# Performance work log

Measured on AMD Instinct MI355X. Metric: run time of the kernel, lower is better.

## Reference

```python
import jax, jax.numpy as jnp
import numpy as np

B, S, H, Q = 32, 128, 128, 3  # users, seq_len, hidden_size, quadkey_level
L = Q - 1  # number of mixing scales


def setup_inputs() -> dict:
    key = jax.random.key(0)
    ks = jax.random.split(key, 12)
    trend0 = jax.random.normal(ks[0], (B, S, H), dtype=jnp.float32)
    trend1 = jax.random.normal(ks[1], (B, S, H), dtype=jnp.float32)
    trend2 = jax.random.normal(ks[2], (B, S, H), dtype=jnp.float32)
    # Per-position prefix linears padded into dense tensors, zero-masked beyond
    # the prefix length j+1 so the ragged math is exact:
    #   W1[j, :j+1, :j+1] ~ Linear(j+1, j+1), b1[j, :j+1]
    #   W2[j, :j+1]      ~ Linear(j+1, 1),   b2[j]
    idx = jnp.arange(S)
    pm = (idx[None, :] <= idx[:, None]).astype(jnp.float32)  # [j, s]: s <= j
    W1 = jax.random.normal(ks[3], (L, S, S, S), dtype=jnp.float32) * 0.05
    W1 = W1 * pm[None, :, :, None] * pm[None, :, None, :]
    b1 = jax.random.normal(ks[4], (L, S, S), dtype=jnp.float32) * 0.05 * pm[None]
    W2 = jax.random.normal(ks[5], (L, S, S), dtype=jnp.float32) * 0.05 * pm[None]
    b2 = jax.random.normal(ks[6], (L, S), dtype=jnp.float32) * 0.05
    # shared output MLP: Linear(H,H)->GELU->Linear(H,H); stored as [in, out]
    Wm1 = jax.random.normal(ks[7], (H, H), dtype=jnp.float32) * 0.05
    bm1 = jax.random.normal(ks[8], (H,), dtype=jnp.float32) * 0.05
    Wm2 = jax.random.normal(ks[9], (H, H), dtype=jnp.float32) * 0.05
    bm2 = jax.random.normal(ks[10], (H,), dtype=jnp.float32) * 0.05
    return {"trend0": trend0, "trend1": trend1, "trend2": trend2,
            "W1": W1, "b1": b1, "W2": W2, "b2": b2,
            "Wm1": Wm1, "bm1": bm1, "Wm2": Wm2, "bm2": bm2}


def reference(trend0, trend1, trend2, W1, b1, W2, b2, Wm1, bm1, Wm2, bm2):
    gelu = lambda x: jax.nn.gelu(x, approximate=False)  # torch nn.GELU default
    mlp = lambda x: gelu(x @ Wm1 + bm1) @ Wm2 + bm2

    rev = [trend2, trend1, trend0]  # trend_list reversed
    out_low = rev[0]
    out_high = rev[1]
    outs = [out_low]
    for i in range(Q - 1):
        # vectorized ragged prefix mix: per position j, out_low[:, :j+1] (as [B,H,j+1])
        # -> Linear(j+1,j+1) -> GELU -> Linear(j+1,1). Zero-padding in W1/b1/W2
        # kills all contributions beyond the prefix (GELU(0)=0).
        y1 = jnp.einsum('bsh,jst->bhjt', out_low, W1[i]) + b1[i]  # [B,H,S,S]
        res = jnp.einsum('bhjt,jt->bjh', gelu(y1), W2[i]) + b2[i][None, :, None]
        out_high = out_high + res
        out_low = out_high
        if i + 2 <= Q - 1:
            out_high = rev[i + 2]
        out_low = mlp(out_low)
        outs.append(out_low)
    outs.reverse()
    return tuple(outs)
```

## Files before the change

### kernel.cpp

```cpp
#include <hip/hip_runtime.h>
#include <stdint.h>

#define BSH (32 * 128 * 128)

typedef __attribute__((ext_vector_type(8))) __bf16 bf16x8;
typedef __attribute__((ext_vector_type(4))) float f32x4;

__device__ __forceinline__ unsigned short f2bf(float f) {
  union { float f; unsigned u; } v; v.f = f;
  return (unsigned short)((v.u + 0x7FFFu + ((v.u >> 16) & 1u)) >> 16);
}

__device__ __forceinline__ float fast_exp2(float x) {
#if __has_builtin(__builtin_amdgcn_exp2f)
  return __builtin_amdgcn_exp2f(x);
#else
  float r; asm("v_exp_f32 %0, %1" : "=v"(r) : "v"(x)); return r;
#endif
}
__device__ __forceinline__ float fast_rcp(float x) {
#if __has_builtin(__builtin_amdgcn_rcpf)
  return __builtin_amdgcn_rcpf(x);
#else
  float r; asm("v_rcp_f32 %0, %1" : "=v"(r) : "v"(x)); return r;
#endif
}

__device__ __forceinline__ float gelu_f(float y) {
  float u = y * y;
  float p = __builtin_fmaf(u, 0.044715f, 1.0f) * y;
  float w = fast_exp2(p * 2.30220787f);
  return y - y * fast_rcp(1.0f + w);
}


__device__ __forceinline__ void transpose_block_c(const float* __restrict__ src,
                                                  unsigned short* __restrict__ dst,
                                                  unsigned short* lds) {
  const int tid = threadIdx.x;
  const float4* s4 = (const float4*)src;
#pragma unroll
  for (int it = 0; it < 16; ++it) {
    int i4 = tid + it * 256;
    float4 v = s4[i4];
    int s = i4 >> 5;
    int t0 = (i4 * 4) & 127;
    int sc = s >> 3, se = s & 7;
#pragma unroll
    for (int e = 0; e < 4; ++e) {
      int t = t0 + e;
      lds[t * 136 + ((sc ^ ((t >> 2) & 7)) << 3) + se] = f2bf(((const float*)&v)[e]);
    }
  }
  __syncthreads();
#pragma unroll
  for (int it = 0; it < 8; ++it) {
    int c = tid + it * 256;
    int tr = c >> 4, sc = c & 15;
    uint4 d = *(const uint4*)(lds + tr * 136 + ((sc ^ ((tr >> 2) & 7)) << 3));
    *(uint4*)(dst + (sc * 128 + tr) * 8) = d;
  }
}

__global__ __launch_bounds__(256) void prepass_kernel(
    const float* __restrict__ W1, const float* __restrict__ trend2,
    const float* __restrict__ Wm1, const float* __restrict__ Wm2,
    unsigned short* __restrict__ W1Tc, unsigned short* __restrict__ T2c,
    unsigned short* __restrict__ Wm1c, unsigned short* __restrict__ Wm2c,
    float* __restrict__ out2) {
  __shared__ unsigned short lds[128 * 136];
  const int bid = blockIdx.x;
  if (bid < 256) {
    transpose_block_c(W1 + bid * 16384, W1Tc + bid * 16384, lds);
  } else if (bid < 288) {
    const int b = bid - 256;
    transpose_block_c(trend2 + b * 16384, T2c + b * 16384, lds);
    const float4* s4 = (const float4*)(trend2 + b * 16384);
    float4* d4 = (float4*)(out2 + b * 16384);
#pragma unroll
    for (int it = 0; it < 16; ++it)
      d4[threadIdx.x + it * 256] = s4[threadIdx.x + it * 256];
  } else if (bid == 288) {
    transpose_block_c(Wm1, Wm1c, lds);
  } else {
    transpose_block_c(Wm2, Wm2c, lds);
  }
}

__global__ __launch_bounds__(256, 4) void mix_kernel(
    const unsigned short* __restrict__ XTc,
    const unsigned short* __restrict__ W1Tc,
    const float* __restrict__ b1,
    const float* __restrict__ W2,
    const float* __restrict__ b2,
    const float* __restrict__ trend,
    unsigned short* __restrict__ xoutc) {
  __shared__ float res_ws[4][4][64];
  const int bid = blockIdx.x;
  const int jg = bid >> 5;
  const int b = bid & 31;
  const int j0 = jg * 4;
  const int tid = threadIdx.x;
  const int wave = tid >> 6;
  const int lane = tid & 63;
  const int lane15 = lane & 15;
  const int quad = lane >> 4;

  const int ntiles = (j0 >> 4) + 1;
  const int ksteps = (j0 >> 5) + 1;

  const unsigned short* Bb = XTc + b * 16384;
  const unsigned short* A0 = W1Tc + j0 * 16384;
  const float C = -2.45546937f;

#pragma unroll
  for (int p = 0; p < 2; ++p) {
    float psum[4][4];
#pragma unroll
    for (int jj = 0; jj < 4; ++jj)
#pragma unroll
      for (int ni = 0; ni < 4; ++ni) psum[jj][ni] = 0.f;

#pragma unroll
    for (int q = 0; q < 2; ++q) {
      const int mt = wave + q * 4;
      if (mt < ntiles) {
        f32x4 acc[4][4];
#pragma unroll
        for (int jj = 0; jj < 4; ++jj)
#pragma unroll
          for (int ni = 0; ni < 4; ++ni) {
            f32x4 z = {0.f, 0.f, 0.f, 0.f};
            acc[jj][ni] = z;
          }
        for (int ks = 0; ks < ksteps; ++ks) {
          const int kq = ks * 4 + quad;
          const unsigned short* bp = Bb + (kq * 128 + p * 64 + lane15) * 8;
          bf16x8 bf0 = *(const bf16x8*)(bp);
          bf16x8 bf1 = *(const bf16x8*)(bp + 128);
          bf16x8 bf2 = *(const bf16x8*)(bp + 256);
          bf16x8 bf3 = *(const bf16x8*)(bp + 384);
#pragma unroll
          for (int jj = 0; jj < 4; ++jj) {
            bf16x8 a = *(const bf16x8*)(A0 + jj * 16384 +
                                        (kq * 128 + mt * 16 + lane15) * 8);
            acc[jj][0] = __builtin_amdgcn_mfma_f32_16x16x32_bf16(a, bf0, acc[jj][0], 0, 0, 0);
            acc[jj][1] = __builtin_amdgcn_mfma_f32_16x16x32_bf16(a, bf1, acc[jj][1], 0, 0, 0);
            acc[jj][2] = __builtin_amdgcn_mfma_f32_16x16x32_bf16(a, bf2, acc[jj][2], 0, 0, 0);
            acc[jj][3] = __builtin_amdgcn_mfma_f32_16x16x32_bf16(a, bf3, acc[jj][3], 0, 0, 0);
          }
        }
        const int tb = mt * 16 + quad * 4;
#pragma unroll
        for (int jj = 0; jj < 4; ++jj) {
          const int j = j0 + jj;
          float4 b1v = *(const float4*)(b1 + j * 128 + tb);
          float4 w2v = *(const float4*)(W2 + j * 128 + tb);
#pragma unroll
          for (int r = 0; r < 4; ++r) {
            float b1r = ((const float*)&b1v)[r];
            float w2r = ((const float*)&w2v)[r];
            float cb = C * b1r;
            float bw = b1r * w2r;
#pragma unroll
            for (int ni = 0; ni < 4; ++ni) {
              float a = acc[jj][ni][r];
              float m = __builtin_fmaf(a, C, cb);
              float e = fast_exp2(m);
              float rr = fast_rcp(1.0f + e);
              float yw = __builtin_fmaf(a, w2r, bw);
              psum[jj][ni] = __builtin_fmaf(yw, rr, psum[jj][ni]);
            }
          }
        }
      }
    }
#pragma unroll
    for (int jj = 0; jj < 4; ++jj)
#pragma unroll
      for (int ni = 0; ni < 4; ++ni) {
        float v = psum[jj][ni];
        v += __shfl_xor(v, 16, 64);
        v += __shfl_xor(v, 32, 64);
        psum[jj][ni] = v;
      }
#pragma unroll
    for (int jj = 0; jj < 4; ++jj)
      res_ws[wave][jj][quad * 16 + lane15] = psum[jj][quad];
    __syncthreads();
    {
      const int jj = tid >> 6;
      const int hh = tid & 63;
      const int j = j0 + jj;
      const int h = p * 64 + hh;
      float v = res_ws[0][jj][hh] + res_ws[1][jj][hh] +
                res_ws[2][jj][hh] + res_ws[3][jj][hh] +
                b2[j] + trend[(b * 128 + j) * 128 + h];
      xoutc[b * 16384 + ((h >> 3) * 128 + j) * 8 + (h & 7)] = f2bf(v);
    }
    __syncthreads();
  }
}

__global__ __launch_bounds__(256) void mlp_kernel(
    const unsigned short* __restrict__ Xc,
    const unsigned short* __restrict__ Wm1c,
    const unsigned short* __restrict__ Wm2c,
    const float* __restrict__ bm1,
    const float* __restrict__ bm2,
    float* __restrict__ outf,
    unsigned short* __restrict__ outTc,
    const int write_t) {
  __shared__ __align__(16) unsigned short U[16 * 128];
  __shared__ unsigned short ldsT[16 * 136];
  const int bid = blockIdx.x;
  const int b = bid >> 3;
  const int mb = bid & 7;
  const int tid = threadIdx.x;
  const int wave = tid >> 6;
  const int lane = tid & 63;
  const int lane15 = lane & 15;
  const int quad = lane >> 4;

  const unsigned short* Xb = Xc + b * 16384;

  f32x4 acc[2];
  { f32x4 z = {0.f, 0.f, 0.f, 0.f}; acc[0] = z; acc[1] = z; }
#pragma unroll
  for (int ks = 0; ks < 4; ++ks) {
    int kq = ks * 4 + quad;
    bf16x8 a  = *(const bf16x8*)(Xb + (kq * 128 + mb * 16 + lane15) * 8);
    bf16x8 w0 = *(const bf16x8*)(Wm1c + (kq * 128 + wave * 32 + lane15) * 8);
    bf16x8 w1 = *(const bf16x8*)(Wm1c + (kq * 128 + wave * 32 + 16 + lane15) * 8);
    acc[0] = __builtin_amdgcn_mfma_f32_16x16x32_bf16(a, w0, acc[0], 0, 0, 0);
    acc[1] = __builtin_amdgcn_mfma_f32_16x16x32_bf16(a, w1, acc[1], 0, 0, 0);
  }
#pragma unroll
  for (int ni = 0; ni < 2; ++ni) {
    int n = wave * 32 + ni * 16 + lane15;
    float bv = bm1[n];
#pragma unroll
    for (int r = 0; r < 4; ++r) {
      int jr = quad * 4 + r;
      U[((n >> 3) * 16 + jr) * 8 + (n & 7)] = f2bf(gelu_f(acc[ni][r] + bv));
    }
  }
  __syncthreads();
  { f32x4 z = {0.f, 0.f, 0.f, 0.f}; acc[0] = z; acc[1] = z; }
#pragma unroll
  for (int ks = 0; ks < 4; ++ks) {
    int kq = ks * 4 + quad;
    bf16x8 a  = *(const bf16x8*)(U + (kq * 16 + lane15) * 8);
    bf16x8 w0 = *(const bf16x8*)(Wm2c + (kq * 128 + wave * 32 + lane15) * 8);
    bf16x8 w1 = *(const bf16x8*)(Wm2c + (kq * 128 + wave * 32 + 16 + lane15) * 8);
    acc[0] = __builtin_amdgcn_mfma_f32_16x16x32_bf16(a, w0, acc[0], 0, 0, 0);
    acc[1] = __builtin_amdgcn_mfma_f32_16x16x32_bf16(a, w1, acc[1], 0, 0, 0);
  }
  {
    float* outb = outf + b * 16384 + mb * 16 * 128;
#pragma unroll
    for (int ni = 0; ni < 2; ++ni) {
      int n = wave * 32 + ni * 16 + lane15;
      float bv = bm2[n];
#pragma unroll
      for (int r = 0; r < 4; ++r) {
        int jr = quad * 4 + r;
        float v = acc[ni][r] + bv;
        outb[jr * 128 + n] = v;
        if (write_t) ldsT[jr * 136 + n] = f2bf(v);
      }
    }
  }
  if (write_t) {
    __syncthreads();
    int h = tid & 127, jr8 = tid >> 7;
    unsigned short tmp[8] __attribute__((aligned(16)));
#pragma unroll
    for (int e = 0; e < 8; ++e) tmp[e] = ldsT[(jr8 * 8 + e) * 136 + h];
    *(uint4*)(outTc + b * 16384 + ((mb * 2 + jr8) * 128 + h) * 8) = *(const uint4*)tmp;
  }
}

extern "C" void kernel_launch(void* const* d_in, const int* in_sizes, int n_in,
                              void* d_out, int out_size, void* d_ws, size_t ws_size,
                              hipStream_t stream) {
  (void)in_sizes; (void)n_in; (void)out_size; (void)ws_size;
  const float* trend0 = (const float*)d_in[0];
  const float* trend1 = (const float*)d_in[1];
  const float* trend2 = (const float*)d_in[2];
  const float* W1  = (const float*)d_in[3];
  const float* b1  = (const float*)d_in[4];
  const float* W2  = (const float*)d_in[5];
  const float* b2  = (const float*)d_in[6];
  const float* Wm1 = (const float*)d_in[7];
  const float* bm1 = (const float*)d_in[8];
  const float* Wm2 = (const float*)d_in[9];
  const float* bm2 = (const float*)d_in[10];
  float* out = (float*)d_out;
  char* ws = (char*)d_ws;

  unsigned short* W1Tc = (unsigned short*)(ws);
  unsigned short* T2c  = (unsigned short*)(ws + 8388608);
  unsigned short* x1c  = (unsigned short*)(ws + 9437184);
  unsigned short* A1Tc = (unsigned short*)(ws + 10485760);
  unsigned short* x2c  = (unsigned short*)(ws + 11534336);
  unsigned short* Wm1c = (unsigned short*)(ws + 12582912);
  unsigned short* Wm2c = (unsigned short*)(ws + 12615680);

  prepass_kernel<<<290, 256, 0, stream>>>(W1, trend2, Wm1, Wm2,
                                          W1Tc, T2c, Wm1c, Wm2c, out + 2 * BSH);
  mix_kernel<<<1024, 256, 0, stream>>>(T2c, W1Tc, b1, W2, b2, trend1, x1c);
  mlp_kernel<<<256, 256, 0, stream>>>(x1c, Wm1c, Wm2c, bm1, bm2,
                                      out + BSH, A1Tc, 1);
  mix_kernel<<<1024, 256, 0, stream>>>(A1Tc, W1Tc + 128 * 16384, b1 + 16384,
                                       W2 + 16384, b2 + 128, trend0, x2c);
  mlp_kernel<<<256, 256, 0, stream>>>(x2c, Wm1c, Wm2c, bm1, bm2,
                                      out, (unsigned short*)nullptr, 0);
}
```

Measured before the change: 146.5 us.

## Fuse output MLP into mix kernel and rebalance ragged block order

Folds the shared output MLP into the mix kernel. Each block keeps its 4 mixed rows in LDS and runs both MLP GEMMs on a 16-row tile that is zero-padded and only 4 rows full, which removes two launches and the intermediate bf16 round trip through global memory. Blocks now map to j-groups in a zig-zag order so the triangular, ragged work is spread more evenly across the grid, and the prepass W1 transpose uses the same ordering. The cost is padded MFMA work on the MLP (only a quarter of each tile is used), smaller output stores, and extra LDS per block, which may affect occupancy.

```diff
diff --git a/kernel.cpp b/kernel.cpp
--- a/kernel.cpp
+++ b/kernel.cpp
@@ -33,6 +33,9 @@
   return y - y * fast_rcp(1.0f + w);
 }
 
+__device__ __forceinline__ int jg_of(int x, int cls) {
+  return cls == 0 ? x : cls == 1 ? 15 - x : cls == 2 ? 16 + x : 31 - x;
+}
 
 __device__ __forceinline__ void transpose_block_c(const float* __restrict__ src,
                                                   unsigned short* __restrict__ dst,
@@ -71,7 +74,11 @@
   __shared__ unsigned short lds[128 * 136];
   const int bid = blockIdx.x;
   if (bid < 256) {
-    transpose_block_c(W1 + bid * 16384, W1Tc + bid * 16384, lds);
+    int x = bid & 7, r = bid >> 3;
+    int stage = r >> 4, rr = r & 15;
+    int j = jg_of(x, rr >> 2) * 4 + (rr & 3);
+    int blk = stage * 128 + j;
+    transpose_block_c(W1 + blk * 16384, W1Tc + blk * 16384, lds);
   } else if (bid < 288) {
     const int b = bid - 256;
     transpose_block_c(trend2 + b * 16384, T2c + b * 16384, lds);
@@ -87,18 +94,28 @@
   }
 }
 
-__global__ __launch_bounds__(256, 4) void mix_kernel(
+__global__ __launch_bounds__(256, 4) void mix_fused_kernel(
     const unsigned short* __restrict__ XTc,
-    const unsigned short* __restrict__ W1Tc,
-    const float* __restrict__ b1,
-    const float* __restrict__ W2,
-    const float* __restrict__ b2,
-    const float* __restrict__ trend,
-    unsigned short* __restrict__ xoutc) {
+    const unsigned short* __restrict__ W1Tj,
+    const float* __restrict__ b1j,
+    const float* __restrict__ W2j,
+    const float* __restrict__ b2j,
+    const float* __restrict__ trendR,
+    const unsigned short* __restrict__ Wm1c,
+    const unsigned short* __restrict__ Wm2c,
+    const float* __restrict__ bm1,
+    const float* __restrict__ bm2,
+    float* __restrict__ outF,
+    unsigned short* __restrict__ outTc,
+    const int write_t) {
   __shared__ float res_ws[4][4][64];
+  __shared__ __align__(16) unsigned short xa[16 * 128];
+  __shared__ __align__(16) unsigned short U[16 * 128];
   const int bid = blockIdx.x;
-  const int jg = bid >> 5;
-  const int b = bid & 31;
+  const int x = bid & 7;
+  const int i = bid >> 3;
+  const int b = i & 31;
+  const int jg = jg_of(x, i >> 5);
   const int j0 = jg * 4;
   const int tid = threadIdx.x;
   const int wave = tid >> 6;
@@ -106,11 +123,16 @@
   const int lane15 = lane & 15;
   const int quad = lane >> 4;
 
+  {
+    uint4 z = {0, 0, 0, 0};
+    ((uint4*)xa)[tid] = z;
+    ((uint4*)U)[tid] = z;
+  }
+
   const int ntiles = (j0 >> 4) + 1;
   const int ksteps = (j0 >> 5) + 1;
-
   const unsigned short* Bb = XTc + b * 16384;
-  const unsigned short* A0 = W1Tc + j0 * 16384;
+  const unsigned short* A0 = W1Tj + j0 * 16384;
   const float C = -2.45546937f;
 
 #pragma unroll
@@ -136,26 +158,27 @@
         for (int ks = 0; ks < ksteps; ++ks) {
           const int kq = ks * 4 + quad;
           const unsigned short* bp = Bb + (kq * 128 + p * 64 + lane15) * 8;
-          bf16x8 bf0 = *(const bf16x8*)(bp);
-          bf16x8 bf1 = *(const bf16x8*)(bp + 128);
-          bf16x8 bf2 = *(const bf16x8*)(bp + 256);
-          bf16x8 bf3 = *(const bf16x8*)(bp + 384);
-#pragma unroll
-          for (int jj = 0; jj < 4; ++jj) {
-            bf16x8 a = *(const bf16x8*)(A0 + jj * 16384 +
-                                        (kq * 128 + mt * 16 + lane15) * 8);
-            acc[jj][0] = __builtin_amdgcn_mfma_f32_16x16x32_bf16(a, bf0, acc[jj][0], 0, 0, 0);
-            acc[jj][1] = __builtin_amdgcn_mfma_f32_16x16x32_bf16(a, bf1, acc[jj][1], 0, 0, 0);
-            acc[jj][2] = __builtin_amdgcn_mfma_f32_16x16x32_bf16(a, bf2, acc[jj][2], 0, 0, 0);
-            acc[jj][3] = __builtin_amdgcn_mfma_f32_16x16x32_bf16(a, bf3, acc[jj][3], 0, 0, 0);
-          }
+          bf16x8 bfr[4], af[4];
+#pragma unroll
+          for (int ni = 0; ni < 4; ++ni)
+            bfr[ni] = *(const bf16x8*)(bp + ni * 128);
+#pragma unroll
+          for (int jj = 0; jj < 4; ++jj)
+            af[jj] = *(const bf16x8*)(A0 + jj * 16384 +
+                                      (kq * 128 + mt * 16 + lane15) * 8);
+#pragma unroll
+          for (int jj = 0; jj < 4; ++jj)
+#pragma unroll
+            for (int ni = 0; ni < 4; ++ni)
+              acc[jj][ni] = __builtin_amdgcn_mfma_f32_16x16x32_bf16(
+                  af[jj], bfr[ni], acc[jj][ni], 0, 0, 0);
         }
         const int tb = mt * 16 + quad * 4;
 #pragma unroll
         for (int jj = 0; jj < 4; ++jj) {
           const int j = j0 + jj;
-          float4 b1v = *(const float4*)(b1 + j * 128 + tb);
-          float4 w2v = *(const float4*)(W2 + j * 128 + tb);
+          float4 b1v = *(const float4*)(b1j + j * 128 + tb);
+          float4 w2v = *(const float4*)(W2j + j * 128 + tb);
 #pragma unroll
           for (int r = 0; r < 4; ++r) {
             float b1r = ((const float*)&b1v)[r];
@@ -167,9 +190,9 @@
               float a = acc[jj][ni][r];
               float m = __builtin_fmaf(a, C, cb);
               float e = fast_exp2(m);
-              float rr = fast_rcp(1.0f + e);
+              float rr2 = fast_rcp(1.0f + e);
               float yw = __builtin_fmaf(a, w2r, bw);
-              psum[jj][ni] = __builtin_fmaf(yw, rr, psum[jj][ni]);
+              psum[jj][ni] = __builtin_fmaf(yw, rr2, psum[jj][ni]);
             }
           }
         }
@@ -195,89 +218,62 @@
       const int h = p * 64 + hh;
       float v = res_ws[0][jj][hh] + res_ws[1][jj][hh] +
                 res_ws[2][jj][hh] + res_ws[3][jj][hh] +
-                b2[j] + trend[(b * 128 + j) * 128 + h];
-      xoutc[b * 16384 + ((h >> 3) * 128 + j) * 8 + (h & 7)] = f2bf(v);
+                b2j[j] + trendR[(b * 128 + j) * 128 + h];
+      xa[((h >> 3) * 16 + jj) * 8 + (h & 7)] = f2bf(v);
     }
     __syncthreads();
   }
-}
-
-__global__ __launch_bounds__(256) void mlp_kernel(
-    const unsigned short* __restrict__ Xc,
-    const unsigned short* __restrict__ Wm1c,
-    const unsigned short* __restrict__ Wm2c,
-    const float* __restrict__ bm1,
-    const float* __restrict__ bm2,
-    float* __restrict__ outf,
-    unsigned short* __restrict__ outTc,
-    const int write_t) {
-  __shared__ __align__(16) unsigned short U[16 * 128];
-  __shared__ unsigned short ldsT[16 * 136];
-  const int bid = blockIdx.x;
-  const int b = bid >> 3;
-  const int mb = bid & 7;
-  const int tid = threadIdx.x;
-  const int wave = tid >> 6;
-  const int lane = tid & 63;
-  const int lane15 = lane & 15;
-  const int quad = lane >> 4;
-
-  const unsigned short* Xb = Xc + b * 16384;
-
-  f32x4 acc[2];
-  { f32x4 z = {0.f, 0.f, 0.f, 0.f}; acc[0] = z; acc[1] = z; }
+
+  f32x4 acc2[2];
+  { f32x4 z = {0.f, 0.f, 0.f, 0.f}; acc2[0] = z; acc2[1] = z; }
 #pragma unroll
   for (int ks = 0; ks < 4; ++ks) {
     int kq = ks * 4 + quad;
-    bf16x8 a  = *(const bf16x8*)(Xb + (kq * 128 + mb * 16 + lane15) * 8);
-    bf16x8 w0 = *(const bf16x8*)(Wm1c + (kq * 128 + wave * 32 + lane15) * 8);
-    bf16x8 w1 = *(const bf16x8*)(Wm1c + (kq * 128 + wave * 32 + 16 + lane15) * 8);
-    acc[0] = __builtin_amdgcn_mfma_f32_16x16x32_bf16(a, w0, acc[0], 0, 0, 0);
-    acc[1] = __builtin_amdgcn_mfma_f32_16x16x32_bf16(a, w1, acc[1], 0, 0, 0);
-  }
-#pragma unroll
-  for (int ni = 0; ni < 2; ++ni) {
-    int n = wave * 32 + ni * 16 + lane15;
-    float bv = bm1[n];
-#pragma unroll
-    for (int r = 0; r < 4; ++r) {
-      int jr = quad * 4 + r;
-      U[((n >> 3) * 16 + jr) * 8 + (n & 7)] = f2bf(gelu_f(acc[ni][r] + bv));
+    bf16x8 a = *(const bf16x8*)(xa + (kq * 16 + lane15) * 8);
+    bf16x8 w0 = *(const bf16x8*)(Wm1c + (kq * 128 + (wave * 2 + 0) * 16 + lane15) * 8);
+    bf16x8 w1 = *(const bf16x8*)(Wm1c + (kq * 128 + (wave * 2 + 1) * 16 + lane15) * 8);
+    acc2[0] = __builtin_amdgcn_mfma_f32_16x16x32_bf16(a, w0, acc2[0], 0, 0, 0);
+    acc2[1] = __builtin_amdgcn_mfma_f32_16x16x32_bf16(a, w1, acc2[1], 0, 0, 0);
+  }
+  if (quad == 0) {
+#pragma unroll
+    for (int nt = 0; nt < 2; ++nt) {
+      int o = (wave * 2 + nt) * 16 + lane15;
+      float bv = bm1[o];
+#pragma unroll
+      for (int r = 0; r < 4; ++r) {
+        float g = gelu_f(acc2[nt][r] + bv);
+        U[((o >> 3) * 16 + r) * 8 + (o & 7)] = f2bf(g);
+      }
     }
   }
   __syncthreads();
-  { f32x4 z = {0.f, 0.f, 0.f, 0.f}; acc[0] = z; acc[1] = z; }
+  { f32x4 z = {0.f, 0.f, 0.f, 0.f}; acc2[0] = z; acc2[1] = z; }
 #pragma unroll
   for (int ks = 0; ks < 4; ++ks) {
     int kq = ks * 4 + quad;
-    bf16x8 a  = *(const bf16x8*)(U + (kq * 16 + lane15) * 8);
-    bf16x8 w0 = *(const bf16x8*)(Wm2c + (kq * 128 + wave * 32 + lane15) * 8);
-    bf16x8 w1 = *(const bf16x8*)(Wm2c + (kq * 128 + wave * 32 + 16 + lane15) * 8);
-    acc[0] = __builtin_amdgcn_mfma_f32_16x16x32_bf16(a, w0, acc[0], 0, 0, 0);
-    acc[1] = __builtin_amdgcn_mfma_f32_16x16x32_bf16(a, w1, acc[1], 0, 0, 0);
-  }
-  {
-    float* outb = outf + b * 16384 + mb * 16 * 128;
-#pragma unroll
-    for (int ni = 0; ni < 2; ++ni) {
-      int n = wave * 32 + ni * 16 + lane15;
-      float bv = bm2[n];
+    bf16x8 a = *(const bf16x8*)(U + (kq * 16 + lane15) * 8);
+    bf16x8 w0 = *(const bf16x8*)(Wm2c + (kq * 128 + (wave * 2 + 0) * 16 + lane15) * 8);
+    bf16x8 w1 = *(const bf16x8*)(Wm2c + (kq * 128 + (wave * 2 + 1) * 16 + lane15) * 8);
+    acc2[0] = __builtin_amdgcn_mfma_f32_16x16x32_bf16(a, w0, acc2[0], 0, 0, 0);
+    acc2[1] = __builtin_amdgcn_mfma_f32_16x16x32_bf16(a, w1, acc2[1], 0, 0, 0);
+  }
+  if (quad == 0) {
+#pragma unroll
+    for (int nt = 0; nt < 2; ++nt) {
+      int o = (wave * 2 + nt) * 16 + lane15;
+      float bv = bm2[o];
+      unsigned short tmp4[4] __attribute__((aligned(8)));
 #pragma unroll
       for (int r = 0; r < 4; ++r) {
-        int jr = quad * 4 + r;
-        float v = acc[ni][r] + bv;
-        outb[jr * 128 + n] = v;
-        if (write_t) ldsT[jr * 136 + n] = f2bf(v);
+        float v = acc2[nt][r] + bv;
+        outF[b * 16384 + (j0 + r) * 128 + o] = v;
+        tmp4[r] = f2bf(v);
       }
-    }
-  }
-  if (write_t) {
-    __syncthreads();
-    int h = tid & 127, jr8 = tid >> 7;
-    unsigned short tmp[8] __attribute__((aligned(16)));
-#pragma unroll
-    for (int e = 0; e < 8; ++e) tmp[e] = ldsT[(jr8 * 8 + e) * 136 + h];
-    *(uint4*)(outTc + b * 16384 + ((mb * 2 + jr8) * 128 + h) * 8) = *(const uint4*)tmp;
+      if (write_t)
+        *(uint2*)(outTc + b * 16384 + ((j0 >> 3) * 128 + o) * 8 + (j0 & 7)) =
+            *(const uint2*)tmp4;
+    }
   }
 }
 
@@ -301,19 +297,16 @@
 
   unsigned short* W1Tc = (unsigned short*)(ws);
   unsigned short* T2c  = (unsigned short*)(ws + 8388608);
-  unsigned short* x1c  = (unsigned short*)(ws + 9437184);
-  unsigned short* A1Tc = (unsigned short*)(ws + 10485760);
-  unsigned short* x2c  = (unsigned short*)(ws + 11534336);
-  unsigned short* Wm1c = (unsigned short*)(ws + 12582912);
-  unsigned short* Wm2c = (unsigned short*)(ws + 12615680);
+  unsigned short* A1Tc = (unsigned short*)(ws + 9437184);
+  unsigned short* Wm1c = (unsigned short*)(ws + 10485760);
+  unsigned short* Wm2c = (unsigned short*)(ws + 10518528);
 
   prepass_kernel<<<290, 256, 0, stream>>>(W1, trend2, Wm1, Wm2,
                                           W1Tc, T2c, Wm1c, Wm2c, out + 2 * BSH);
-  mix_kernel<<<1024, 256, 0, stream>>>(T2c, W1Tc, b1, W2, b2, trend1, x1c);
-  mlp_kernel<<<256, 256, 0, stream>>>(x1c, Wm1c, Wm2c, bm1, bm2,
-                                      out + BSH, A1Tc, 1);
-  mix_kernel<<<1024, 256, 0, stream>>>(A1Tc, W1Tc + 128 * 16384, b1 + 16384,
-                                       W2 + 16384, b2 + 128, trend0, x2c);
-  mlp_kernel<<<256, 256, 0, stream>>>(x2c, Wm1c, Wm2c, bm1, bm2,
-                                      out, (unsigned short*)nullptr, 0);
-}
+  mix_fused_kernel<<<1024, 256, 0, stream>>>(
+      T2c, W1Tc, b1, W2, b2, trend1, Wm1c, Wm2c, bm1, bm2,
+      out + BSH, A1Tc, 1);
+  mix_fused_kernel<<<1024, 256, 0, stream>>>(
+      A1Tc, W1Tc + 128 * 16384, b1 + 16384, W2 + 16384, b2 + 128, trend0,
+      Wm1c, Wm2c, bm1, bm2, out, (unsigned short*)nullptr, 0);
+}
```

Result: no change. 145.8 us (-0.5%).

## Pair small and large prefix positions per block to balance triangular mix work

Applied to the files above, without the earlier changes.

The mix kernel now gives each 128-thread block one batch and a pair of positions j and 127-j, so every block carries roughly the same amount of triangular work. Each wave owns one half of the hidden dimension and loops over all M tiles itself, which removes the cross-wave LDS reduction and the __syncthreads. The prepass also reorders which W1 blocks each workgroup transposes, pairing small and large positions there as well. In exchange the per-block parallelism is lower, since each wave iterates serially over up to eight tiles, and more blocks are launched.

```diff
diff --git a/kernel.cpp b/kernel.cpp
--- a/kernel.cpp
+++ b/kernel.cpp
@@ -32,7 +32,6 @@
   float w = fast_exp2(p * 2.30220787f);
   return y - y * fast_rcp(1.0f + w);
 }
-
 
 __device__ __forceinline__ void transpose_block_c(const float* __restrict__ src,
                                                   unsigned short* __restrict__ dst,
@@ -71,7 +70,13 @@
   __shared__ unsigned short lds[128 * 136];
   const int bid = blockIdx.x;
   if (bid < 256) {
-    transpose_block_c(W1 + bid * 16384, W1Tc + bid * 16384, lds);
+    int x = bid & 7, i = bid >> 3;
+    int stage = i >> 4, u = i & 15;
+    int m = u & 7, half = u >> 3;
+    int jpp = x + 8 * m;
+    int j = half ? 127 - jpp : jpp;
+    int blk = stage * 128 + j;
+    transpose_block_c(W1 + blk * 16384, W1Tc + blk * 16384, lds);
   } else if (bid < 288) {
     const int b = bid - 256;
     transpose_block_c(trend2 + b * 16384, T2c + b * 16384, lds);
@@ -87,118 +92,116 @@
   }
 }
 
-__global__ __launch_bounds__(256, 4) void mix_kernel(
+__global__ __launch_bounds__(128, 4) void mix_kernel(
     const unsigned short* __restrict__ XTc,
-    const unsigned short* __restrict__ W1Tc,
-    const float* __restrict__ b1,
-    const float* __restrict__ W2,
-    const float* __restrict__ b2,
-    const float* __restrict__ trend,
+    const unsigned short* __restrict__ W1Tj,
+    const float* __restrict__ b1j,
+    const float* __restrict__ W2j,
+    const float* __restrict__ b2j,
+    const float* __restrict__ trendR,
     unsigned short* __restrict__ xoutc) {
-  __shared__ float res_ws[4][4][64];
   const int bid = blockIdx.x;
-  const int jg = bid >> 5;
-  const int b = bid & 31;
-  const int j0 = jg * 4;
+  const int b = bid >> 6;
+  const int jp = bid & 63;
+  const int js = jp, jb = 127 - jp;
   const int tid = threadIdx.x;
-  const int wave = tid >> 6;
+  const int p = tid >> 6;
   const int lane = tid & 63;
   const int lane15 = lane & 15;
   const int quad = lane >> 4;
 
-  const int ntiles = (j0 >> 4) + 1;
-  const int ksteps = (j0 >> 5) + 1;
-
-  const unsigned short* Bb = XTc + b * 16384;
-  const unsigned short* A0 = W1Tc + j0 * 16384;
+  const int nt_s = (js >> 4) + 1, ks_s = (js >> 5) + 1;
+  const int nt_b = (jb >> 4) + 1, ks_b = (jb >> 5) + 1;
+
+  const unsigned short* Bp = XTc + b * 16384 + (p * 64 + lane15) * 8;
+  const unsigned short* As = W1Tj + js * 16384 + lane15 * 8;
+  const unsigned short* Ab = W1Tj + jb * 16384 + lane15 * 8;
   const float C = -2.45546937f;
 
-#pragma unroll
-  for (int p = 0; p < 2; ++p) {
-    float psum[4][4];
-#pragma unroll
-    for (int jj = 0; jj < 4; ++jj)
-#pragma unroll
-      for (int ni = 0; ni < 4; ++ni) psum[jj][ni] = 0.f;
-
-#pragma unroll
-    for (int q = 0; q < 2; ++q) {
-      const int mt = wave + q * 4;
-      if (mt < ntiles) {
-        f32x4 acc[4][4];
-#pragma unroll
-        for (int jj = 0; jj < 4; ++jj)
-#pragma unroll
-          for (int ni = 0; ni < 4; ++ni) {
-            f32x4 z = {0.f, 0.f, 0.f, 0.f};
-            acc[jj][ni] = z;
-          }
-        for (int ks = 0; ks < ksteps; ++ks) {
-          const int kq = ks * 4 + quad;
-          const unsigned short* bp = Bb + (kq * 128 + p * 64 + lane15) * 8;
-          bf16x8 bf0 = *(const bf16x8*)(bp);
-          bf16x8 bf1 = *(const bf16x8*)(bp + 128);
-          bf16x8 bf2 = *(const bf16x8*)(bp + 256);
-          bf16x8 bf3 = *(const bf16x8*)(bp + 384);
-#pragma unroll
-          for (int jj = 0; jj < 4; ++jj) {
-            bf16x8 a = *(const bf16x8*)(A0 + jj * 16384 +
-                                        (kq * 128 + mt * 16 + lane15) * 8);
-            acc[jj][0] = __builtin_amdgcn_mfma_f32_16x16x32_bf16(a, bf0, acc[jj][0], 0, 0, 0);
-            acc[jj][1] = __builtin_amdgcn_mfma_f32_16x16x32_bf16(a, bf1, acc[jj][1], 0, 0, 0);
-            acc[jj][2] = __builtin_amdgcn_mfma_f32_16x16x32_bf16(a, bf2, acc[jj][2], 0, 0, 0);
-            acc[jj][3] = __builtin_amdgcn_mfma_f32_16x16x32_bf16(a, bf3, acc[jj][3], 0, 0, 0);
-          }
+  float psum[2][4];
+#pragma unroll
+  for (int jj = 0; jj < 2; ++jj)
+#pragma unroll
+    for (int ni = 0; ni < 4; ++ni) psum[jj][ni] = 0.f;
+
+  for (int mt = 0; mt < nt_b; ++mt) {
+    const bool in_s = (mt < nt_s);
+    f32x4 acc[2][4];
+#pragma unroll
+    for (int jj = 0; jj < 2; ++jj)
+#pragma unroll
+      for (int ni = 0; ni < 4; ++ni) {
+        f32x4 z = {0.f, 0.f, 0.f, 0.f};
+        acc[jj][ni] = z;
+      }
+    const int mo = mt * 128;
+    for (int ks = 0; ks < ks_b; ++ks) {
+      const int ko = (ks * 4 + quad) * 1024;
+      bf16x8 vb0 = *(const bf16x8*)(Bp + ko);
+      bf16x8 vb1 = *(const bf16x8*)(Bp + ko + 128);
+      bf16x8 vb2 = *(const bf16x8*)(Bp + ko + 256);
+      bf16x8 vb3 = *(const bf16x8*)(Bp + ko + 384);
+      bf16x8 ab = *(const bf16x8*)(Ab + ko + mo);
+      acc[1][0] = __builtin_amdgcn_mfma_f32_16x16x32_bf16(ab, vb0, acc[1][0], 0, 0, 0);
+      acc[1][1] = __builtin_amdgcn_mfma_f32_16x16x32_bf16(ab, vb1, acc[1][1], 0, 0, 0);
+      acc[1][2] = __builtin_amdgcn_mfma_f32_16x16x32_bf16(ab, vb2, acc[1][2], 0, 0, 0);
+      acc[1][3] = __builtin_amdgcn_mfma_f32_16x16x32_bf16(ab, vb3, acc[1][3], 0, 0, 0);
+      if (in_s && ks < ks_s) {
+        bf16x8 as = *(const bf16x8*)(As + ko + mo);
+        acc[0][0] = __builtin_amdgcn_mfma_f32_16x16x32_bf16(as, vb0, acc[0][0], 0, 0, 0);
+        acc[0][1] = __builtin_amdgcn_mfma_f32_16x16x32_bf16(as, vb1, acc[0][1], 0, 0, 0);
+        acc[0][2] = __builtin_amdgcn_mfma_f32_16x16x32_bf16(as, vb2, acc[0][2], 0, 0, 0);
+        acc[0][3] = __builtin_amdgcn_mfma_f32_16x16x32_bf16(as, vb3, acc[0][3], 0, 0, 0);
+      }
+    }
+    const int tb = mt * 16 + quad * 4;
+#pragma unroll
+    for (int jj = 0; jj < 2; ++jj) {
+      if (jj == 0 && !in_s) continue;
+      const int j = jj ? jb : js;
+      float4 b1v = *(const float4*)(b1j + j * 128 + tb);
+      float4 w2v = *(const float4*)(W2j + j * 128 + tb);
+#pragma unroll
+      for (int r = 0; r < 4; ++r) {
+        float b1r = ((const float*)&b1v)[r];
+        float w2r = ((const float*)&w2v)[r];
+        float cb = C * b1r;
+        float bw = b1r * w2r;
+#pragma unroll
+        for (int ni = 0; ni < 4; ++ni) {
+          float a = acc[jj][ni][r];
+          float m = __builtin_fmaf(a, C, cb);
+          float e = fast_exp2(m);
+          float rr2 = fast_rcp(1.0f + e);
+          float yw = __builtin_fmaf(a, w2r, bw);
+          psum[jj][ni] = __builtin_fmaf(yw, rr2, psum[jj][ni]);
         }
-        const int tb = mt * 16 + quad * 4;
-#pragma unroll
-        for (int jj = 0; jj < 4; ++jj) {
-          const int j = j0 + jj;
-          float4 b1v = *(const float4*)(b1 + j * 128 + tb);
-          float4 w2v = *(const float4*)(W2 + j * 128 + tb);
-#pragma unroll
-          for (int r = 0; r < 4; ++r) {
-            float b1r = ((const float*)&b1v)[r];
-            float w2r = ((const float*)&w2v)[r];
-            float cb = C * b1r;
-            float bw = b1r * w2r;
-#pragma unroll
-            for (int ni = 0; ni < 4; ++ni) {
-              float a = acc[jj][ni][r];
-              float m = __builtin_fmaf(a, C, cb);
-              float e = fast_exp2(m);
-              float rr = fast_rcp(1.0f + e);
-              float yw = __builtin_fmaf(a, w2r, bw);
-              psum[jj][ni] = __builtin_fmaf(yw, rr, psum[jj][ni]);
-            }
-          }
-        }
-      }
-    }
-#pragma unroll
-    for (int jj = 0; jj < 4; ++jj)
+      }
+    }
+  }
+
+#pragma unroll
+  for (int jj = 0; jj < 2; ++jj)
+#pragma unroll
+    for (int ni = 0; ni < 4; ++ni) {
+      float v = psum[jj][ni];
+      v += __shfl_xor(v, 16, 64);
+      v += __shfl_xor(v, 32, 64);
+      psum[jj][ni] = v;
+    }
+
+  if (quad == 0) {
+#pragma unroll
+    for (int jj = 0; jj < 2; ++jj) {
+      const int j = jj ? jb : js;
+      const float bias = b2j[j];
 #pragma unroll
       for (int ni = 0; ni < 4; ++ni) {
-        float v = psum[jj][ni];
-        v += __shfl_xor(v, 16, 64);
-        v += __shfl_xor(v, 32, 64);
-        psum[jj][ni] = v;
-      }
-#pragma unroll
-    for (int jj = 0; jj < 4; ++jj)
-      res_ws[wave][jj][quad * 16 + lane15] = psum[jj][quad];
-    __syncthreads();
-    {
-      const int jj = tid >> 6;
-      const int hh = tid & 63;
-      const int j = j0 + jj;
-      const int h = p * 64 + hh;
-      float v = res_ws[0][jj][hh] + res_ws[1][jj][hh] +
-                res_ws[2][jj][hh] + res_ws[3][jj][hh] +
-                b2[j] + trend[(b * 128 + j) * 128 + h];
-      xoutc[b * 16384 + ((h >> 3) * 128 + j) * 8 + (h & 7)] = f2bf(v);
-    }
-    __syncthreads();
+        const int h = p * 64 + ni * 16 + lane15;
+        float v = psum[jj][ni] + bias + trendR[(b * 128 + j) * 128 + h];
+        xoutc[b * 16384 + ((h >> 3) * 128 + j) * 8 + (h & 7)] = f2bf(v);
+      }
+    }
   }
 }
 
@@ -309,10 +312,10 @@
 
   prepass_kernel<<<290, 256, 0, stream>>>(W1, trend2, Wm1, Wm2,
                                           W1Tc, T2c, Wm1c, Wm2c, out + 2 * BSH);
-  mix_kernel<<<1024, 256, 0, stream>>>(T2c, W1Tc, b1, W2, b2, trend1, x1c);
+  mix_kernel<<<2048, 128, 0, stream>>>(T2c, W1Tc, b1, W2, b2, trend1, x1c);
   mlp_kernel<<<256, 256, 0, stream>>>(x1c, Wm1c, Wm2c, bm1, bm2,
                                       out + BSH, A1Tc, 1);
-  mix_kernel<<<1024, 256, 0, stream>>>(A1Tc, W1Tc + 128 * 16384, b1 + 16384,
+  mix_kernel<<<2048, 128, 0, stream>>>(A1Tc, W1Tc + 128 * 16384, b1 + 16384,
                                        W2 + 16384, b2 + 128, trend0, x2c);
   mlp_kernel<<<256, 256, 0, stream>>>(x2c, Wm1c, Wm2c, bm1, bm2,
                                       out, (unsigned short*)nullptr, 0);
```

After: 152.7 us. 4.3% more time.
